# Optimization experiments

Hardware: AMD Instinct MI355X
Metric: run time of the kernel (lower is better)

Reference implementation:

```python
import jax, jax.numpy as jnp
import numpy as np

N_NODES = 50000
N_EDGES = 600000
N_GRAPHS = 64
D_NODE = 64
D_EDGE = 16
HID = 128
N_LAYERS = 3
LN_EPS = 1e-5


def setup_inputs() -> dict:
    key = jax.random.key(0)
    ks = jax.random.split(key, 16)
    inp = {
        'x': jax.random.normal(ks[0], (N_NODES, D_NODE), dtype=jnp.float32),
        'edge_index': jax.random.randint(ks[1], (2, N_EDGES), 0, N_NODES, dtype=jnp.int64),
        'edge_attr': jax.random.normal(ks[2], (N_EDGES, D_EDGE), dtype=jnp.float32),
        'batch': jnp.sort(jax.random.randint(ks[3], (N_NODES,), 0, N_GRAPHS, dtype=jnp.int64)),
    }
    def lin(k, fan_in, fan_out):
        bound = 1.0 / np.sqrt(fan_in)
        kw, kb = jax.random.split(k)
        w = jax.random.uniform(kw, (fan_in, fan_out), minval=-bound, maxval=bound, dtype=jnp.float32)
        b = jax.random.uniform(kb, (fan_out,), minval=-bound, maxval=bound, dtype=jnp.float32)
        return w, b
    inp['enc_w'], inp['enc_b'] = lin(ks[4], D_NODE, HID)
    inp['ln_g'] = jnp.ones((HID,), jnp.float32)
    inp['ln_b'] = jnp.zeros((HID,), jnp.float32)
    inp['edge_w'], inp['edge_b'] = lin(ks[5], D_EDGE, HID // 2)
    cw, cb = [], []
    for i in range(N_LAYERS):
        w, b = lin(ks[6 + i], HID, HID)
        cw.append(w); cb.append(b)
    inp['conv_ws'] = jnp.stack(cw)  # [L, HID, HID]
    inp['conv_bs'] = jnp.stack(cb)  # [L, HID]
    inp['c1_w'], inp['c1_b'] = lin(ks[10], HID, HID // 2)
    inp['c2_w'], inp['c2_b'] = lin(ks[11], HID // 2, 1)
    return inp


def _layernorm(h, g, b):
    mu = jnp.mean(h, axis=-1, keepdims=True)
    var = jnp.mean(jnp.square(h - mu), axis=-1, keepdims=True)
    return (h - mu) * jax.lax.rsqrt(var + LN_EPS) * g + b


def _gcn_forward(x, edge_attr, batch, src, dst,
                 enc_w, enc_b, ln_g, ln_b, edge_w, edge_b,
                 conv_ws, conv_bs, c1_w, c1_b, c2_w, c2_b):
    # node encoder: Linear -> ReLU -> LayerNorm
    h = _layernorm(jax.nn.relu(x @ enc_w + enc_b), ln_g, ln_b)
    # edge encoder (output unused downstream, kept for fidelity)
    _ = jax.nn.relu(edge_attr @ edge_w + edge_b)
    # GCN normalization with self-loops: deg = in-degree + 1
    deg = jax.ops.segment_sum(jnp.ones((src.shape[0],), h.dtype), dst, num_segments=N_NODES) + 1.0
    dis = jax.lax.rsqrt(deg)  # deg >= 1
    edge_norm = (dis[src] * dis[dst])[:, None]
    self_norm = (dis * dis)[:, None]  # 1/deg for self-loop
    for i in range(N_LAYERS):
        hw = h @ conv_ws[i]
        agg = jax.ops.segment_sum(hw[src] * edge_norm, dst, num_segments=N_NODES)
        h = agg + hw * self_norm + conv_bs[i]
        h = jax.nn.relu(h)  # dropout is identity at eval
    # global mean pool over graphs
    sums = jax.ops.segment_sum(h, batch, num_segments=N_GRAPHS)
    cnts = jax.ops.segment_sum(jnp.ones((h.shape[0],), h.dtype), batch, num_segments=N_GRAPHS)
    pooled = sums / jnp.maximum(cnts, 1.0)[:, None]
    # classifier: Linear -> ReLU -> (Dropout) -> Linear
    return jax.nn.relu(pooled @ c1_w + c1_b) @ c2_w + c2_b


def reference(x, edge_index, edge_attr, batch, enc_w, enc_b, ln_g, ln_b,
              edge_w, edge_b, conv_ws, conv_bs, c1_w, c1_b, c2_w, c2_b):
    src, dst = edge_index[0], edge_index[1]
    return _gcn_forward(x, edge_attr, batch, src, dst, enc_w, enc_b, ln_g, ln_b,
                        edge_w, edge_b, conv_ws, conv_bs, c1_w, c1_b, c2_w, c2_b)
```

## Files before the change

kernel.cpp:

```cpp
#include <hip/hip_runtime.h>

#define HID 128
#define DNODE 64
#define NNODES 50000
#define NEDGES 600000
#define NGRAPHS 64
#define LN_EPS 1e-5f
#define SCAN_BLK 256
#define NSCAN ((NNODES + SCAN_BLK - 1) / SCAN_BLK)

#define NZERO (NNODES + NGRAPHS * HID)
#define NZERO4 (NZERO / 4)
#define Z_BLKS ((NZERO4 + 255) / 256)
#define PKWC_BLKS (3 * 16384 / 256)
#define PKWE_BLKS (8192 / 256)
#define BND_BLKS ((NNODES + 255) / 256)

#define CNT_BLKS ((NEDGES + 255) / 256)
#define ENC_BLKS ((NNODES + 63) / 64)
#define FILL_BLKS ((NEDGES + 255) / 256)

#define GC_BLKS (NNODES / 16)

typedef __attribute__((ext_vector_type(8))) short bf16x8;
typedef __attribute__((ext_vector_type(8))) unsigned short u16x8;
typedef __attribute__((ext_vector_type(4))) float f32x4;
typedef __attribute__((ext_vector_type(2))) float f32x2;

static __device__ __forceinline__ unsigned short f2bf(float f) {
  unsigned int u = __float_as_uint(f);
  u += 0x7fffu + ((u >> 16) & 1u);
  return (unsigned short)(u >> 16);
}
static __device__ __forceinline__ float bf2f(unsigned short h) {
  return __uint_as_float(((unsigned int)h) << 16);
}
static __device__ __forceinline__ void fp8x4_to_f32(unsigned int w, float* o) {
  f32x2 lo = __builtin_amdgcn_cvt_pk_f32_fp8(w, false);
  f32x2 hi = __builtin_amdgcn_cvt_pk_f32_fp8(w, true);
  o[0] = lo[0]; o[1] = lo[1]; o[2] = hi[0]; o[3] = hi[1];
}
static __device__ __forceinline__ unsigned int f32x4_to_fp8(float a, float b,
                                                            float c, float d) {
  unsigned int v = __builtin_amdgcn_cvt_pk_fp8_f32(a, b, 0, false);
  v = __builtin_amdgcn_cvt_pk_fp8_f32(c, d, v, true);
  return v;
}

__global__ void __launch_bounds__(256) prep0_kernel(
    int4* __restrict__ zp, const float* __restrict__ W,
    unsigned short* __restrict__ Wp, const float* __restrict__ enc_w,
    unsigned short* __restrict__ Wpe, const int* __restrict__ batch,
    int* __restrict__ gstart, int* __restrict__ gend) {
  int b = blockIdx.x;
  if (b < Z_BLKS) {
    int i = b * 256 + threadIdx.x;
    if (i < NZERO4) zp[i] = make_int4(0, 0, 0, 0);
  } else if (b < Z_BLKS + PKWC_BLKS) {
    int t = (b - Z_BLKS) * 256 + threadIdx.x;
    int i = t & 7;
    int lane = (t >> 3) & 63;
    int kk = (t >> 9) & 3;
    int nt = (t >> 11) & 7;
    int layer = t >> 14;
    int k = kk * 32 + (lane >> 4) * 8 + i;
    int n = nt * 16 + (lane & 15);
    Wp[t] = f2bf(W[((size_t)layer * HID + k) * HID + n]);
  } else if (b < Z_BLKS + PKWC_BLKS + PKWE_BLKS) {
    int t = (b - Z_BLKS - PKWC_BLKS) * 256 + threadIdx.x;
    int i = t & 7;
    int lane = (t >> 3) & 63;
    int kk = (t >> 9) & 1;
    int nt = (t >> 10) & 7;
    int k = kk * 32 + (lane >> 4) * 8 + i;
    int n = nt * 16 + (lane & 15);
    Wpe[t] = f2bf(enc_w[(size_t)k * HID + n]);
  } else {
    int i = (b - Z_BLKS - PKWC_BLKS - PKWE_BLKS) * 256 + threadIdx.x;
    if (i < NNODES) {
      int g = batch[i];
      if (i == 0 || batch[i - 1] != g) gstart[g] = i;
      if (i == NNODES - 1 || batch[i + 1] != g) gend[g] = i + 1;
    }
  }
}

__global__ void __launch_bounds__(256) prep1_kernel(
    const float* __restrict__ x, const unsigned short* __restrict__ Wpe,
    const unsigned short* __restrict__ Wp0, const float* __restrict__ enc_b,
    const float* __restrict__ ln_g, const float* __restrict__ ln_b,
    unsigned char* __restrict__ B1, const int* __restrict__ dst,
    int* __restrict__ degi, int* __restrict__ erank) {
  __shared__ __align__(16) unsigned short tile[4][16][136];
  int blk = blockIdx.x;
  if (blk < CNT_BLKS) {
    int e = blk * 256 + threadIdx.x;
    if (e < NEDGES) erank[e] = atomicAdd(&degi[dst[e]], 1);
    return;
  }
  int b2 = blk - CNT_BLKS;
  int wave = threadIdx.x >> 6;
  int lane = threadIdx.x & 63;
  int l15 = lane & 15, h = lane >> 4;
  int base = b2 * 64 + wave * 16;
  int row = base + l15;
  int rowc = row < NNODES ? row : NNODES - 1;
  const float* xr = x + (size_t)rowc * DNODE;
  bf16x8 a[2];
#pragma unroll
  for (int kk = 0; kk < 2; ++kk) {
    float4 p0 = *(const float4*)(xr + kk * 32 + h * 8);
    float4 p1 = *(const float4*)(xr + kk * 32 + h * 8 + 4);
    a[kk][0] = (short)f2bf(p0.x); a[kk][1] = (short)f2bf(p0.y);
    a[kk][2] = (short)f2bf(p0.z); a[kk][3] = (short)f2bf(p0.w);
    a[kk][4] = (short)f2bf(p1.x); a[kk][5] = (short)f2bf(p1.y);
    a[kk][6] = (short)f2bf(p1.z); a[kk][7] = (short)f2bf(p1.w);
  }
  f32x4 acc[8];
#pragma unroll
  for (int nt = 0; nt < 8; ++nt) acc[nt] = (f32x4)(0.f);
  const bf16x8* wp = (const bf16x8*)Wpe;
#pragma unroll
  for (int kk = 0; kk < 2; ++kk)
#pragma unroll
    for (int nt = 0; nt < 8; ++nt)
      acc[nt] = __builtin_amdgcn_mfma_f32_16x16x32_bf16(a[kk], wp[(nt * 2 + kk) * 64 + lane],
                                                        acc[nt], 0, 0, 0);
  float s[4] = {0.f, 0.f, 0.f, 0.f}, s2[4] = {0.f, 0.f, 0.f, 0.f};
#pragma unroll
  for (int nt = 0; nt < 8; ++nt) {
    float bcol = enc_b[nt * 16 + l15];
#pragma unroll
    for (int r = 0; r < 4; ++r) {
      float v = fmaxf(acc[nt][r] + bcol, 0.f);
      acc[nt][r] = v;
      s[r] += v;
      s2[r] = fmaf(v, v, s2[r]);
    }
  }
#pragma unroll
  for (int r = 0; r < 4; ++r) {
#pragma unroll
    for (int o = 1; o < 16; o <<= 1) {
      s[r] += __shfl_xor(s[r], o);
      s2[r] += __shfl_xor(s2[r], o);
    }
  }
  float mu[4], rstd[4];
#pragma unroll
  for (int r = 0; r < 4; ++r) {
    mu[r] = s[r] * (1.0f / HID);
    float var = s2[r] * (1.0f / HID) - mu[r] * mu[r];
    rstd[r] = rsqrtf(var + LN_EPS);
  }
#pragma unroll
  for (int nt = 0; nt < 8; ++nt) {
    float gcol = ln_g[nt * 16 + l15], bbcol = ln_b[nt * 16 + l15];
#pragma unroll
    for (int r = 0; r < 4; ++r)
      tile[wave][h * 4 + r][nt * 16 + l15] =
          f2bf((acc[nt][r] - mu[r]) * rstd[r] * gcol + bbcol);
  }
  __syncthreads();
  bf16x8 a2[4];
#pragma unroll
  for (int kk = 0; kk < 4; ++kk)
    a2[kk] = *(const bf16x8*)&tile[wave][l15][kk * 32 + h * 8];
  __syncthreads();
  f32x4 acc2[8];
#pragma unroll
  for (int nt = 0; nt < 8; ++nt) acc2[nt] = (f32x4)(0.f);
#pragma unroll
  for (int kk = 0; kk < 4; ++kk) {
#pragma unroll
    for (int nt = 0; nt < 8; ++nt) {
      bf16x8 wf = *(const bf16x8*)(Wp0 + (((nt * 4 + kk) * 64 + lane) << 3));
      acc2[nt] = __builtin_amdgcn_mfma_f32_16x16x32_bf16(a2[kk], wf, acc2[nt], 0, 0, 0);
    }
  }
#pragma unroll
  for (int nt = 0; nt < 8; ++nt)
#pragma unroll
    for (int r = 0; r < 4; ++r)
      tile[wave][h * 4 + r][nt * 16 + l15] = f2bf(acc2[nt][r]);
  __syncthreads();
  int trow = lane >> 2, tseg = lane & 3;
  int orow = base + trow;
  if (orow < NNODES) {
#pragma unroll
    for (int q = 0; q < 4; ++q) {
      u16x8 v = *(const u16x8*)&tile[wave][trow][tseg * 32 + q * 8];
      uint2 o;
      o.x = f32x4_to_fp8(bf2f((unsigned short)v[0]), bf2f((unsigned short)v[1]),
                         bf2f((unsigned short)v[2]), bf2f((unsigned short)v[3]));
      o.y = f32x4_to_fp8(bf2f((unsigned short)v[4]), bf2f((unsigned short)v[5]),
                         bf2f((unsigned short)v[6]), bf2f((unsigned short)v[7]));
      *(uint2*)(B1 + (size_t)orow * HID + tseg * 32 + q * 8) = o;
    }
  }
}

__global__ void __launch_bounds__(SCAN_BLK) blocksum_kernel(
    const int* __restrict__ degi, int* __restrict__ bsum) {
  int i = blockIdx.x * SCAN_BLK + threadIdx.x;
  int v = (i < NNODES) ? degi[i] : 0;
#pragma unroll
  for (int off = 32; off; off >>= 1) v += __shfl_down(v, off);
  __shared__ int wsum[4];
  if ((threadIdx.x & 63) == 0) wsum[threadIdx.x >> 6] = v;
  __syncthreads();
  if (threadIdx.x == 0) bsum[blockIdx.x] = wsum[0] + wsum[1] + wsum[2] + wsum[3];
}

__global__ void __launch_bounds__(SCAN_BLK) offsets_kernel(
    const int* __restrict__ degi, const int* __restrict__ bsum,
    int* __restrict__ off, float* __restrict__ dis) {
  int b = blockIdx.x, t = threadIdx.x;
  __shared__ int sb[SCAN_BLK];
  __shared__ int s[SCAN_BLK];
  __shared__ int wred[4];
  sb[t] = (t < NSCAN) ? bsum[t] : 0;
  __syncthreads();
  int v = (t < b) ? sb[t] : 0;
#pragma unroll
  for (int o = 32; o; o >>= 1) v += __shfl_down(v, o);
  if ((t & 63) == 0) wred[t >> 6] = v;
  __syncthreads();
  int base = wred[0] + wred[1] + wred[2] + wred[3];
  int i = b * SCAN_BLK + t;
  int dv = (i < NNODES) ? degi[i] : 0;
  s[t] = dv;
  __syncthreads();
  for (int d = 1; d < SCAN_BLK; d <<= 1) {
    int x = (t >= d) ? s[t - d] : 0;
    __syncthreads();
    s[t] += x;
    __syncthreads();
  }
  if (i < NNODES) {
    int excl = s[t] - dv + base;
    off[i] = excl;
    dis[i] = rsqrtf((float)dv + 1.0f);
  }
  if (b == 0 && t == 0) off[NNODES] = NEDGES;
}

__global__ void __launch_bounds__(256) fill_kernel(
    const int* __restrict__ src, const int* __restrict__ dst,
    const int* __restrict__ erank, const int* __restrict__ off,
    const float* __restrict__ dis, unsigned int* __restrict__ epack) {
  int e = blockIdx.x * 256 + threadIdx.x;
  if (e >= NEDGES) return;
  int d = dst[e];
  int sN = src[e];
  int r = erank[e];
  epack[off[d] + r] =
      ((unsigned int)f2bf(dis[sN] * dis[d]) << 16) | (unsigned int)sN;
}

__global__ void __launch_bounds__(1024) gc_kernel(
    const int* __restrict__ off, const unsigned int* __restrict__ epack,
    const float* __restrict__ dis, const float* __restrict__ bias,
    const unsigned char* __restrict__ Bin, const unsigned short* __restrict__ Wnext,
    unsigned char* __restrict__ Bout) {
  __shared__ __align__(16) unsigned short As[16][136];
  __shared__ __align__(16) unsigned short Bs[16][136];
  int w = threadIdx.x >> 6, lane = threadIdx.x & 63;
  int n = blockIdx.x * 16 + w;
  int slot = lane >> 4, p = lane & 15;
  int lo = off[n], hi = off[n + 1];
  float acc0[8], acc1[8];
#pragma unroll
  for (int i = 0; i < 8; ++i) { acc0[i] = 0.f; acc1[i] = 0.f; }
  int idx = lo + slot;
  for (; idx + 4 < hi; idx += 8) {
    unsigned int e0 = epack[idx];
    unsigned int e1 = epack[idx + 4];
    float w0 = bf2f((unsigned short)(e0 >> 16));
    float w1 = bf2f((unsigned short)(e1 >> 16));
    uint2 v0 = *(const uint2*)(Bin + (size_t)(e0 & 0xFFFFu) * HID + p * 8);
    uint2 v1 = *(const uint2*)(Bin + (size_t)(e1 & 0xFFFFu) * HID + p * 8);
    float f0[8], f1[8];
    fp8x4_to_f32(v0.x, f0); fp8x4_to_f32(v0.y, f0 + 4);
    fp8x4_to_f32(v1.x, f1); fp8x4_to_f32(v1.y, f1 + 4);
#pragma unroll
    for (int i = 0; i < 8; ++i) acc0[i] = fmaf(f0[i], w0, acc0[i]);
#pragma unroll
    for (int i = 0; i < 8; ++i) acc1[i] = fmaf(f1[i], w1, acc1[i]);
  }
  if (idx < hi) {
    unsigned int e0 = epack[idx];
    float w0 = bf2f((unsigned short)(e0 >> 16));
    uint2 v0 = *(const uint2*)(Bin + (size_t)(e0 & 0xFFFFu) * HID + p * 8);
    float f0[8];
    fp8x4_to_f32(v0.x, f0); fp8x4_to_f32(v0.y, f0 + 4);
#pragma unroll
    for (int i = 0; i < 8; ++i) acc0[i] = fmaf(f0[i], w0, acc0[i]);
  }
#pragma unroll
  for (int i = 0; i < 8; ++i) {
    float a = acc0[i] + acc1[i];
    a += __shfl_xor(a, 16);
    a += __shfl_xor(a, 32);
    acc0[i] = a;
  }
  if (slot == 0) {
    float dn = dis[n];
    float d2 = dn * dn;
    uint2 sv = *(const uint2*)(Bin + (size_t)n * HID + p * 8);
    float sf[8];
    fp8x4_to_f32(sv.x, sf); fp8x4_to_f32(sv.y, sf + 4);
    float4 b0 = ((const float4*)bias)[p * 2];
    float4 b1 = ((const float4*)bias)[p * 2 + 1];
    float bb[8] = {b0.x, b0.y, b0.z, b0.w, b1.x, b1.y, b1.z, b1.w};
    u16x8 o;
#pragma unroll
    for (int i = 0; i < 8; ++i) {
      float v = fmaxf(fmaf(sf[i], d2, bb[i]) + acc0[i], 0.f);
      o[i] = (short)f2bf(v);
    }
    *(u16x8*)&As[w][p * 8] = o;
  }
  __syncthreads();
  if (w < 8) {
    bf16x8 a[4];
#pragma unroll
    for (int kk = 0; kk < 4; ++kk)
      a[kk] = *(const bf16x8*)&As[p][kk * 32 + slot * 8];
    f32x4 acc = (f32x4)(0.f);
#pragma unroll
    for (int kk = 0; kk < 4; ++kk) {
      bf16x8 wf = *(const bf16x8*)(Wnext + (((w * 4 + kk) * 64 + lane) << 3));
      acc = __builtin_amdgcn_mfma_f32_16x16x32_bf16(a[kk], wf, acc, 0, 0, 0);
    }
#pragma unroll
    for (int r = 0; r < 4; ++r)
      Bs[slot * 4 + r][w * 16 + p] = f2bf(acc[r]);
  }
  __syncthreads();
  if (threadIdx.x < 256) {
    int row = threadIdx.x >> 4, seg = threadIdx.x & 15;
    u16x8 v = *(const u16x8*)&Bs[row][seg * 8];
    uint2 o;
    o.x = f32x4_to_fp8(bf2f((unsigned short)v[0]), bf2f((unsigned short)v[1]),
                       bf2f((unsigned short)v[2]), bf2f((unsigned short)v[3]));
    o.y = f32x4_to_fp8(bf2f((unsigned short)v[4]), bf2f((unsigned short)v[5]),
                       bf2f((unsigned short)v[6]), bf2f((unsigned short)v[7]));
    *(uint2*)(Bout + (size_t)(blockIdx.x * 16 + row) * HID + seg * 8) = o;
  }
}

__global__ void __launch_bounds__(1024) g2pool_kernel(
    const int* __restrict__ off, const unsigned int* __restrict__ epack,
    const float* __restrict__ dis, const float* __restrict__ bias,
    const unsigned char* __restrict__ Bin, const int* __restrict__ batch,
    float* __restrict__ sums) {
  __shared__ float Ps[16][132];
  __shared__ int bg[16];
  int w = threadIdx.x >> 6, lane = threadIdx.x & 63;
  int n = blockIdx.x * 16 + w;
  int slot = lane >> 4, p = lane & 15;
  int lo = off[n], hi = off[n + 1];
  float acc0[8], acc1[8];
#pragma unroll
  for (int i = 0; i < 8; ++i) { acc0[i] = 0.f; acc1[i] = 0.f; }
  int idx = lo + slot;
  for (; idx + 4 < hi; idx += 8) {
    unsigned int e0 = epack[idx];
    unsigned int e1 = epack[idx + 4];
    float w0 = bf2f((unsigned short)(e0 >> 16));
    float w1 = bf2f((unsigned short)(e1 >> 16));
    uint2 v0 = *(const uint2*)(Bin + (size_t)(e0 & 0xFFFFu) * HID + p * 8);
    uint2 v1 = *(const uint2*)(Bin + (size_t)(e1 & 0xFFFFu) * HID + p * 8);
    float f0[8], f1[8];
    fp8x4_to_f32(v0.x, f0); fp8x4_to_f32(v0.y, f0 + 4);
    fp8x4_to_f32(v1.x, f1); fp8x4_to_f32(v1.y, f1 + 4);
#pragma unroll
    for (int i = 0; i < 8; ++i) acc0[i] = fmaf(f0[i], w0, acc0[i]);
#pragma unroll
    for (int i = 0; i < 8; ++i) acc1[i] = fmaf(f1[i], w1, acc1[i]);
  }
  if (idx < hi) {
    unsigned int e0 = epack[idx];
    float w0 = bf2f((unsigned short)(e0 >> 16));
    uint2 v0 = *(const uint2*)(Bin + (size_t)(e0 & 0xFFFFu) * HID + p * 8);
    float f0[8];
    fp8x4_to_f32(v0.x, f0); fp8x4_to_f32(v0.y, f0 + 4);
#pragma unroll
    for (int i = 0; i < 8; ++i) acc0[i] = fmaf(f0[i], w0, acc0[i]);
  }
#pragma unroll
  for (int i = 0; i < 8; ++i) {
    float a = acc0[i] + acc1[i];
    a += __shfl_xor(a, 16);
    a += __shfl_xor(a, 32);
    acc0[i] = a;
  }
  if (slot == 0) {
    float dn = dis[n];
    float d2 = dn * dn;
    uint2 sv = *(const uint2*)(Bin + (size_t)n * HID + p * 8);
    float sf[8];
    fp8x4_to_f32(sv.x, sf); fp8x4_to_f32(sv.y, sf + 4);
    float4 b0 = ((const float4*)bias)[p * 2];
    float4 b1 = ((const float4*)bias)[p * 2 + 1];
    float bb[8] = {b0.x, b0.y, b0.z, b0.w, b1.x, b1.y, b1.z, b1.w};
    float4 o0, o1;
    o0.x = fmaxf(fmaf(sf[0], d2, bb[0]) + acc0[0], 0.f);
    o0.y = fmaxf(fmaf(sf[1], d2, bb[1]) + acc0[1], 0.f);
    o0.z = fmaxf(fmaf(sf[2], d2, bb[2]) + acc0[2], 0.f);
    o0.w = fmaxf(fmaf(sf[3], d2, bb[3]) + acc0[3], 0.f);
    o1.x = fmaxf(fmaf(sf[4], d2, bb[4]) + acc0[4], 0.f);
    o1.y = fmaxf(fmaf(sf[5], d2, bb[5]) + acc0[5], 0.f);
    o1.z = fmaxf(fmaf(sf[6], d2, bb[6]) + acc0[6], 0.f);
    o1.w = fmaxf(fmaf(sf[7], d2, bb[7]) + acc0[7], 0.f);
    *(float4*)&Ps[w][p * 8] = o0;
    *(float4*)&Ps[w][p * 8 + 4] = o1;
  }
  if (threadIdx.x < 16) bg[threadIdx.x] = batch[blockIdx.x * 16 + threadIdx.x];
  __syncthreads();
  if (threadIdx.x < HID) {
    int j = threadIdx.x;
    float a = 0.f;
    int cur = bg[0];
    for (int r = 0; r < 16; ++r) {
      int g = bg[r];
      if (g != cur) { atomicAdd(&sums[cur * HID + j], a); a = 0.f; cur = g; }
      a += Ps[r][j];
    }
    atomicAdd(&sums[cur * HID + j], a);
  }
}

__global__ void __launch_bounds__(64) cls_kernel(
    const float* __restrict__ sums, const int* __restrict__ gstart,
    const int* __restrict__ gend, const float* __restrict__ c1w,
    const float* __restrict__ c1b, const float* __restrict__ c2w,
    const float* __restrict__ c2b, float* __restrict__ out) {
  int g = blockIdx.x;
  int j = threadIdx.x;
  __shared__ float pooled[HID];
  float cnt = (float)(gend[g] - gstart[g]);
  float inv = 1.0f / fmaxf(cnt, 1.0f);
  pooled[j] = sums[g * HID + j] * inv;
  pooled[j + 64] = sums[g * HID + j + 64] * inv;
  __syncthreads();
  float s = c1b[j];
#pragma unroll 8
  for (int k = 0; k < HID; ++k) s = fmaf(pooled[k], c1w[k * 64 + j], s);
  s = fmaxf(s, 0.f) * c2w[j];
#pragma unroll
  for (int off = 32; off; off >>= 1) s += __shfl_down(s, off);
  if (j == 0) out[g] = s + c2b[0];
}

extern "C" void kernel_launch(void* const* d_in, const int* in_sizes, int n_in,
                              void* d_out, int out_size, void* d_ws, size_t ws_size,
                              hipStream_t stream) {
  const float* x = (const float*)d_in[0];
  const int* edge_index = (const int*)d_in[1];
  const int* batch = (const int*)d_in[3];
  const float* enc_w = (const float*)d_in[4];
  const float* enc_b = (const float*)d_in[5];
  const float* ln_g = (const float*)d_in[6];
  const float* ln_b = (const float*)d_in[7];
  const float* conv_ws = (const float*)d_in[10];
  const float* conv_bs = (const float*)d_in[11];
  const float* c1w = (const float*)d_in[12];
  const float* c1b = (const float*)d_in[13];
  const float* c2w = (const float*)d_in[14];
  const float* c2b = (const float*)d_in[15];
  float* out = (float*)d_out;

  unsigned char* B1 = (unsigned char*)d_ws;
  unsigned char* B2 = B1 + (size_t)NNODES * HID;
  unsigned short* Wp = (unsigned short*)(B2 + (size_t)NNODES * HID);
  unsigned short* Wpe = Wp + 3 * 16384;
  unsigned int* epack = (unsigned int*)(Wpe + 8192);
  int* erank = (int*)(epack + NEDGES);
  int* degi = erank + NEDGES;
  float* sums = (float*)(degi + NNODES);
  int* off = (int*)(sums + NGRAPHS * HID);
  float* dis = (float*)(off + NNODES + 1);
  int* bsum = (int*)(dis + NNODES);
  int* gstart = bsum + SCAN_BLK;
  int* gend = gstart + NGRAPHS;

  const int* srcp = edge_index;
  const int* dstp = edge_index + NEDGES;

  prep0_kernel<<<Z_BLKS + PKWC_BLKS + PKWE_BLKS + BND_BLKS, 256, 0, stream>>>(
      (int4*)degi, conv_ws, Wp, enc_w, Wpe, batch, gstart, gend);
  prep1_kernel<<<CNT_BLKS + ENC_BLKS, 256, 0, stream>>>(
      x, Wpe, Wp, enc_b, ln_g, ln_b, B1, dstp, degi, erank);
  blocksum_kernel<<<NSCAN, SCAN_BLK, 0, stream>>>(degi, bsum);
  offsets_kernel<<<NSCAN, SCAN_BLK, 0, stream>>>(degi, bsum, off, dis);
  fill_kernel<<<FILL_BLKS, 256, 0, stream>>>(srcp, dstp, erank, off, dis, epack);

  gc_kernel<<<GC_BLKS, 1024, 0, stream>>>(off, epack, dis, conv_bs, B1,
                                          Wp + (size_t)1 * 16384, B2);
  gc_kernel<<<GC_BLKS, 1024, 0, stream>>>(off, epack, dis, conv_bs + HID, B2,
                                          Wp + (size_t)2 * 16384, B1);
  g2pool_kernel<<<GC_BLKS, 1024, 0, stream>>>(off, epack, dis, conv_bs + 2 * HID,
                                              B1, batch, sums);
  cls_kernel<<<NGRAPHS, 64, 0, stream>>>(sums, gstart, gend, c1w, c1b, c2w, c2b, out);
}
```

Baseline: 167.9 us.

## Replace per-node atomic CSR build with two-level bucket sort of edges

The CSR construction no longer counts degrees with one global atomic per edge. Edges are now bucketed by dst>>6 using shared-memory histograms and a single-block scan, scattered into buckets, and then sorted within each bucket by a block that also writes node offsets and degree norms. A separate pass computes the per-edge normalisation. This cuts global atomic contention, but it adds kernels and extra passes over the edge arrays, and the within-bucket order of edges is no longer deterministic.

```diff
diff --git a/kernel.cpp b/kernel.cpp
--- a/kernel.cpp
+++ b/kernel.cpp
@@ -6,19 +6,20 @@
 #define NEDGES 600000
 #define NGRAPHS 64
 #define LN_EPS 1e-5f
-#define SCAN_BLK 256
-#define NSCAN ((NNODES + SCAN_BLK - 1) / SCAN_BLK)
-
-#define NZERO (NNODES + NGRAPHS * HID)
-#define NZERO4 (NZERO / 4)
+
+#define NBUCK 782
+#define EPB 4096
+#define BK1 ((NEDGES + EPB - 1) / EPB)
+
+#define NZERO (NBUCK + NGRAPHS * HID)
+#define NZERO4 ((NZERO + 3) / 4)
 #define Z_BLKS ((NZERO4 + 255) / 256)
 #define PKWC_BLKS (3 * 16384 / 256)
 #define PKWE_BLKS (8192 / 256)
 #define BND_BLKS ((NNODES + 255) / 256)
 
-#define CNT_BLKS ((NEDGES + 255) / 256)
 #define ENC_BLKS ((NNODES + 63) / 64)
-#define FILL_BLKS ((NEDGES + 255) / 256)
+#define E256_BLKS ((NEDGES + 255) / 256)
 
 #define GC_BLKS (NNODES / 16)
 
@@ -90,15 +91,45 @@
     const unsigned short* __restrict__ Wp0, const float* __restrict__ enc_b,
     const float* __restrict__ ln_g, const float* __restrict__ ln_b,
     unsigned char* __restrict__ B1, const int* __restrict__ dst,
-    int* __restrict__ degi, int* __restrict__ erank) {
+    int* __restrict__ gcount, unsigned int* __restrict__ bpos) {
   __shared__ __align__(16) unsigned short tile[4][16][136];
+  __shared__ int lhist[NBUCK];
   int blk = blockIdx.x;
-  if (blk < CNT_BLKS) {
-    int e = blk * 256 + threadIdx.x;
-    if (e < NEDGES) erank[e] = atomicAdd(&degi[dst[e]], 1);
+  if (blk < BK1) {
+    int t = threadIdx.x;
+    for (int i = t; i < NBUCK; i += 256) lhist[i] = 0;
+    __syncthreads();
+    int base = blk * EPB;
+    int myd[16];
+    int myr[16];
+#pragma unroll
+    for (int i = 0; i < 16; ++i) {
+      int e = base + i * 256 + t;
+      if (e < NEDGES) {
+        int d = dst[e];
+        myd[i] = d;
+        myr[i] = atomicAdd(&lhist[d >> 6], 1);
+      } else {
+        myd[i] = -1;
+        myr[i] = 0;
+      }
+    }
+    __syncthreads();
+    for (int i = t; i < NBUCK; i += 256) {
+      int c = lhist[i];
+      if (c) lhist[i] = atomicAdd(&gcount[i], c);
+    }
+    __syncthreads();
+#pragma unroll
+    for (int i = 0; i < 16; ++i) {
+      if (myd[i] >= 0) {
+        int e = base + i * 256 + t;
+        bpos[e] = (unsigned int)(lhist[myd[i] >> 6] + myr[i]);
+      }
+    }
     return;
   }
-  int b2 = blk - CNT_BLKS;
+  int b2 = blk - BK1;
   int wave = threadIdx.x >> 6;
   int lane = threadIdx.x & 63;
   int l15 = lane & 15, h = lane >> 4;
@@ -200,62 +231,80 @@
   }
 }
 
-__global__ void __launch_bounds__(SCAN_BLK) blocksum_kernel(
-    const int* __restrict__ degi, int* __restrict__ bsum) {
-  int i = blockIdx.x * SCAN_BLK + threadIdx.x;
-  int v = (i < NNODES) ? degi[i] : 0;
-#pragma unroll
-  for (int off = 32; off; off >>= 1) v += __shfl_down(v, off);
-  __shared__ int wsum[4];
-  if ((threadIdx.x & 63) == 0) wsum[threadIdx.x >> 6] = v;
-  __syncthreads();
-  if (threadIdx.x == 0) bsum[blockIdx.x] = wsum[0] + wsum[1] + wsum[2] + wsum[3];
-}
-
-__global__ void __launch_bounds__(SCAN_BLK) offsets_kernel(
-    const int* __restrict__ degi, const int* __restrict__ bsum,
-    int* __restrict__ off, float* __restrict__ dis) {
+__global__ void __launch_bounds__(1024) scan_kernel(
+    const int* __restrict__ gcount, int* __restrict__ boff,
+    int* __restrict__ off) {
+  __shared__ int s[1024];
+  int t = threadIdx.x;
+  int v = (t < NBUCK) ? gcount[t] : 0;
+  s[t] = v;
+  __syncthreads();
+  for (int d = 1; d < 1024; d <<= 1) {
+    int xv = (t >= d) ? s[t - d] : 0;
+    __syncthreads();
+    s[t] += xv;
+    __syncthreads();
+  }
+  if (t < NBUCK) boff[t] = s[t] - v;
+  if (t == 0) {
+    boff[NBUCK] = s[1023];
+    off[NNODES] = NEDGES;
+  }
+}
+
+__global__ void __launch_bounds__(256) scat_kernel(
+    const int* __restrict__ src, const int* __restrict__ dst,
+    const unsigned int* __restrict__ bpos, const int* __restrict__ boff,
+    unsigned int* __restrict__ sorted1) {
+  int e = blockIdx.x * 256 + threadIdx.x;
+  if (e >= NEDGES) return;
+  int d = dst[e];
+  unsigned int u = ((unsigned int)d << 16) | (unsigned int)src[e];
+  sorted1[boff[d >> 6] + bpos[e]] = u;
+}
+
+__global__ void __launch_bounds__(1024) bucket_kernel(
+    const int* __restrict__ boff, const unsigned int* __restrict__ sorted1,
+    int* __restrict__ off, float* __restrict__ dis,
+    unsigned int* __restrict__ epack) {
+  __shared__ int h64[64];
+  __shared__ int cur[64];
   int b = blockIdx.x, t = threadIdx.x;
-  __shared__ int sb[SCAN_BLK];
-  __shared__ int s[SCAN_BLK];
-  __shared__ int wred[4];
-  sb[t] = (t < NSCAN) ? bsum[t] : 0;
-  __syncthreads();
-  int v = (t < b) ? sb[t] : 0;
-#pragma unroll
-  for (int o = 32; o; o >>= 1) v += __shfl_down(v, o);
-  if ((t & 63) == 0) wred[t >> 6] = v;
-  __syncthreads();
-  int base = wred[0] + wred[1] + wred[2] + wred[3];
-  int i = b * SCAN_BLK + t;
-  int dv = (i < NNODES) ? degi[i] : 0;
-  s[t] = dv;
-  __syncthreads();
-  for (int d = 1; d < SCAN_BLK; d <<= 1) {
-    int x = (t >= d) ? s[t - d] : 0;
-    __syncthreads();
-    s[t] += x;
-    __syncthreads();
-  }
-  if (i < NNODES) {
-    int excl = s[t] - dv + base;
-    off[i] = excl;
-    dis[i] = rsqrtf((float)dv + 1.0f);
-  }
-  if (b == 0 && t == 0) off[NNODES] = NEDGES;
-}
-
-__global__ void __launch_bounds__(256) fill_kernel(
-    const int* __restrict__ src, const int* __restrict__ dst,
-    const int* __restrict__ erank, const int* __restrict__ off,
+  int lo = boff[b], hi = boff[b + 1];
+  if (t < 64) h64[t] = 0;
+  __syncthreads();
+  for (int i = lo + t; i < hi; i += 1024)
+    atomicAdd(&h64[(sorted1[i] >> 16) & 63], 1);
+  __syncthreads();
+  if (t == 0) {
+    int run = 0;
+    for (int j = 0; j < 64; ++j) {
+      int c = h64[j];
+      cur[j] = lo + run;
+      int n = b * 64 + j;
+      if (n < NNODES) {
+        off[n] = lo + run;
+        dis[n] = rsqrtf((float)c + 1.0f);
+      }
+      run += c;
+    }
+  }
+  __syncthreads();
+  for (int i = lo + t; i < hi; i += 1024) {
+    unsigned int u = sorted1[i];
+    int p = atomicAdd(&cur[(u >> 16) & 63], 1);
+    epack[p] = u;
+  }
+}
+
+__global__ void __launch_bounds__(256) norm_kernel(
     const float* __restrict__ dis, unsigned int* __restrict__ epack) {
   int e = blockIdx.x * 256 + threadIdx.x;
   if (e >= NEDGES) return;
-  int d = dst[e];
-  int sN = src[e];
-  int r = erank[e];
-  epack[off[d] + r] =
-      ((unsigned int)f2bf(dis[sN] * dis[d]) << 16) | (unsigned int)sN;
+  unsigned int u = epack[e];
+  int d = u >> 16;
+  int sN = u & 0xFFFFu;
+  epack[e] = ((unsigned int)f2bf(dis[sN] * dis[d]) << 16) | (unsigned int)sN;
 }
 
 __global__ void __launch_bounds__(1024) gc_kernel(
@@ -477,25 +526,27 @@
   unsigned short* Wp = (unsigned short*)(B2 + (size_t)NNODES * HID);
   unsigned short* Wpe = Wp + 3 * 16384;
   unsigned int* epack = (unsigned int*)(Wpe + 8192);
-  int* erank = (int*)(epack + NEDGES);
-  int* degi = erank + NEDGES;
-  float* sums = (float*)(degi + NNODES);
-  int* off = (int*)(sums + NGRAPHS * HID);
+  unsigned int* sorted1 = epack + NEDGES;
+  unsigned int* bpos = sorted1 + NEDGES;
+  int* gcount = (int*)(bpos + NEDGES);
+  float* sums = (float*)(gcount + NBUCK);
+  int* boff = (int*)(sums + NGRAPHS * HID);
+  int* off = boff + NBUCK + 1;
   float* dis = (float*)(off + NNODES + 1);
-  int* bsum = (int*)(dis + NNODES);
-  int* gstart = bsum + SCAN_BLK;
+  int* gstart = (int*)(dis + NNODES);
   int* gend = gstart + NGRAPHS;
 
   const int* srcp = edge_index;
   const int* dstp = edge_index + NEDGES;
 
   prep0_kernel<<<Z_BLKS + PKWC_BLKS + PKWE_BLKS + BND_BLKS, 256, 0, stream>>>(
-      (int4*)degi, conv_ws, Wp, enc_w, Wpe, batch, gstart, gend);
-  prep1_kernel<<<CNT_BLKS + ENC_BLKS, 256, 0, stream>>>(
-      x, Wpe, Wp, enc_b, ln_g, ln_b, B1, dstp, degi, erank);
-  blocksum_kernel<<<NSCAN, SCAN_BLK, 0, stream>>>(degi, bsum);
-  offsets_kernel<<<NSCAN, SCAN_BLK, 0, stream>>>(degi, bsum, off, dis);
-  fill_kernel<<<FILL_BLKS, 256, 0, stream>>>(srcp, dstp, erank, off, dis, epack);
+      (int4*)gcount, conv_ws, Wp, enc_w, Wpe, batch, gstart, gend);
+  prep1_kernel<<<BK1 + ENC_BLKS, 256, 0, stream>>>(
+      x, Wpe, Wp, enc_b, ln_g, ln_b, B1, dstp, gcount, bpos);
+  scan_kernel<<<1, 1024, 0, stream>>>(gcount, boff, off);
+  scat_kernel<<<E256_BLKS, 256, 0, stream>>>(srcp, dstp, bpos, boff, sorted1);
+  bucket_kernel<<<NBUCK, 1024, 0, stream>>>(boff, sorted1, off, dis, epack);
+  norm_kernel<<<E256_BLKS, 256, 0, stream>>>(dis, epack);
 
   gc_kernel<<<GC_BLKS, 1024, 0, stream>>>(off, epack, dis, conv_bs, B1,
                                           Wp + (size_t)1 * 16384, B2);
```

Result: faster. 158.5 us (-5.6%).
